# Kernel optimization log

Measured on AMD Instinct MI355X. Metric: run time of the kernel, lower is better.

Reference implementation:

```python
import jax, jax.numpy as jnp
import numpy as np

EPS = 1e-06  # slot-attention renorm epsilon
LN_EPS = 1e-05  # torch LayerNorm default
NUM_ITERS = 3


def layernorm(x, w, b):
    m = jnp.mean(x, axis=-1, keepdims=True)
    v = jnp.mean((x - m) ** 2, axis=-1, keepdims=True)
    return (x - m) * jax.lax.rsqrt(v + LN_EPS) * w + b


def setup_inputs() -> dict:
    key = jax.random.key(0)
    ks = jax.random.split(key, 16)
    B, N, D = 32, 4096, 512
    S, NS, H = 128, 8, 256
    def lin(k, out_f, in_f):
        return jax.random.normal(k, (out_f, in_f), jnp.float32) * (1.0 / np.sqrt(in_f))
    return {
        "inputs": jax.random.normal(ks[0], (B, N, D), jnp.float32),
        "slots_init": jax.random.normal(ks[1], (B, NS, S), jnp.float32),
        "ln_in_w": jnp.ones((D,), jnp.float32), "ln_in_b": jnp.zeros((D,), jnp.float32),
        "ln_slot_w": jnp.ones((S,), jnp.float32), "ln_slot_b": jnp.zeros((S,), jnp.float32),
        "ln_mlp_w": jnp.ones((S,), jnp.float32), "ln_mlp_b": jnp.zeros((S,), jnp.float32),
        "Wq": lin(ks[2], S, S), "Wk": lin(ks[3], S, D), "Wv": lin(ks[4], S, D),
        "gru_Wih": lin(ks[5], 3 * S, S), "gru_Whh": lin(ks[6], 3 * S, S),
        "gru_bih": jnp.zeros((3 * S,), jnp.float32), "gru_bhh": jnp.zeros((3 * S,), jnp.float32),
        "mlp_W1": lin(ks[7], H, S), "mlp_b1": jnp.zeros((H,), jnp.float32),
        "mlp_W2": lin(ks[8], S, H), "mlp_b2": jnp.zeros((S,), jnp.float32),
        "slots_mu": jax.random.normal(ks[9], (1, 1, S), jnp.float32) * 0.1,
        "slots_log_sigma": jax.random.normal(ks[10], (1, 1, S), jnp.float32) * 0.1,
    }


def gru_cell(x, h, Wih, Whh, bih, bhh):
    # PyTorch GRUCell math. x, h: [BS, S]
    S = h.shape[-1]
    gi = x @ Wih.T + bih
    gh = h @ Whh.T + bhh
    i_r, i_z, i_n = gi[:, :S], gi[:, S:2 * S], gi[:, 2 * S:]
    h_r, h_z, h_n = gh[:, :S], gh[:, S:2 * S], gh[:, 2 * S:]
    r = jax.nn.sigmoid(i_r + h_r)
    z = jax.nn.sigmoid(i_z + h_z)
    n = jnp.tanh(i_n + r * h_n)
    return (1.0 - z) * n + z * h


def reference(inputs, slots_init, ln_in_w, ln_in_b, ln_slot_w, ln_slot_b, ln_mlp_w, ln_mlp_b,
              Wq, Wk, Wv, gru_Wih, gru_Whh, gru_bih, gru_bhh,
              mlp_W1, mlp_b1, mlp_W2, mlp_b2, slots_mu, slots_log_sigma):
    B, N, D = inputs.shape
    NS, S = slots_init.shape[1], slots_init.shape[2]
    x = layernorm(inputs, ln_in_w, ln_in_b)
    k = jnp.einsum('bnd,sd->bns', x, Wk)  # [B,N,S]
    v = jnp.einsum('bnd,sd->bns', x, Wv)
    slots = slots_mu + jnp.exp(slots_log_sigma) * slots_init  # [B,NS,S]
    scale = S ** (-0.5)
    for _ in range(NUM_ITERS):
        slots_prev = slots
        q = jnp.einsum('bmd,sd->bms', layernorm(slots, ln_slot_w, ln_slot_b), Wq)  # [B,NS,S]
        attn_logits = scale * jnp.einsum('bns,bms->bnm', k, q)  # [B,N,NS]
        attn = jax.nn.softmax(attn_logits, axis=-1) + EPS
        attn = attn / jnp.sum(attn, axis=1, keepdims=True)  # normalize over inputs
        updates = jnp.einsum('bnm,bns->bms', attn, v)  # [B,NS,S]
        h = gru_cell(updates.reshape(B * NS, S), slots_prev.reshape(B * NS, S),
                     gru_Wih, gru_Whh, gru_bih, gru_bhh).reshape(B, NS, S)
        mlp_out = jnp.maximum(layernorm(h, ln_mlp_w, ln_mlp_b) @ mlp_W1.T + mlp_b1, 0.0) @ mlp_W2.T + mlp_b2
        slots = h + mlp_out
    return slots
```

## Files before the change

kernel.cpp:

```cpp
#include <hip/hip_runtime.h>

typedef __bf16 v8bf __attribute__((ext_vector_type(8)));
typedef __bf16 v4bf __attribute__((ext_vector_type(4)));
typedef float  v4f  __attribute__((ext_vector_type(4)));
typedef unsigned short u16;

#define LN_EPS_F 1e-5f
#define ATTN_EPS 1e-6f

static constexpr int Bsz = 32;
static constexpr int Nn  = 4096;
static constexpr int Dd  = 512;
static constexpr int Ss  = 128;
static constexpr int NSs = 8;
static constexpr int Hh  = 256;
static constexpr int MROWS = Bsz * Nn;

__device__ __forceinline__ void load_lds16(const void* g, void* l) {
    __builtin_amdgcn_global_load_lds(
        (const __attribute__((address_space(1))) void*)g,
        (__attribute__((address_space(3))) void*)l, 16, 0, 0);
}

__global__ __launch_bounds__(256) void k_cast(const float* __restrict__ X,
                                              u16* __restrict__ Xb,
                                              float2* __restrict__ stats) {
    const int wid = threadIdx.x >> 6, lane = threadIdx.x & 63;
    const int row = blockIdx.x * 4 + wid;
    const float4* xp = reinterpret_cast<const float4*>(X + (size_t)row * Dd) + lane * 2;
    float4 a = xp[0];
    float4 b = xp[1];
    float s  = a.x + a.y + a.z + a.w + b.x + b.y + b.z + b.w;
    float s2 = a.x*a.x + a.y*a.y + a.z*a.z + a.w*a.w
             + b.x*b.x + b.y*b.y + b.z*b.z + b.w*b.w;
    v8bf o;
    o[0] = (__bf16)a.x; o[1] = (__bf16)a.y; o[2] = (__bf16)a.z; o[3] = (__bf16)a.w;
    o[4] = (__bf16)b.x; o[5] = (__bf16)b.y; o[6] = (__bf16)b.z; o[7] = (__bf16)b.w;
    *reinterpret_cast<v8bf*>(Xb + (size_t)row * Dd + lane * 8) = o;
#pragma unroll
    for (int off = 32; off > 0; off >>= 1) {
        s  += __shfl_xor(s, off);
        s2 += __shfl_xor(s2, off);
    }
    if (lane == 0) {
        float m = s * (1.0f / Dd);
        float v = s2 * (1.0f / Dd) - m * m;
        stats[row] = make_float2(m, rsqrtf(v + LN_EPS_F));
    }
}

__global__ __launch_bounds__(256) void k_prep(const float* __restrict__ Wk, const float* __restrict__ Wv,
                                              const float* __restrict__ ln_in_w, const float* __restrict__ ln_in_b,
                                              const float* __restrict__ slots_init, const float* __restrict__ mu,
                                              const float* __restrict__ lsig,
                                              u16* __restrict__ Wkvp, float* __restrict__ cb,
                                              float* __restrict__ Scol, float* __restrict__ slots) {
    const int bid = blockIdx.x;
    const int t = threadIdx.x;
    if (bid < 512) {
        int idx = bid * 256 + t;
        int n = idx >> 9, d = idx & 511;
        float w = (n < Ss) ? Wk[n * Dd + d] : Wv[(n - Ss) * Dd + d];
        w *= ln_in_w[d];
        __bf16 bv = (__bf16)w;
        Wkvp[idx] = __builtin_bit_cast(u16, bv);
    } else if (bid < 640) {
        int idx = (bid - 512) * 256 + t;
        int sidx = idx & (Ss - 1);
        slots[idx] = mu[sidx] + expf(lsig[sidx]) * slots_init[idx];
    } else {
        const int wid = t >> 6, lane = t & 63;
        const int rowbase = (bid - 640) * 32 + wid * 8;
        const int d0 = lane * 8;
        float4 lw0 = *reinterpret_cast<const float4*>(ln_in_w + d0);
        float4 lw1 = *reinterpret_cast<const float4*>(ln_in_w + d0 + 4);
        float4 lb0 = *reinterpret_cast<const float4*>(ln_in_b + d0);
        float4 lb1 = *reinterpret_cast<const float4*>(ln_in_b + d0 + 4);
        for (int rr = 0; rr < 8; ++rr) {
            int row = rowbase + rr;
            const float* wrow = (row < Ss) ? (Wk + (size_t)row * Dd)
                                           : (Wv + (size_t)(row - Ss) * Dd);
            float4 w0 = *reinterpret_cast<const float4*>(wrow + d0);
            float4 w1 = *reinterpret_cast<const float4*>(wrow + d0 + 4);
            float accb = lb0.x*w0.x + lb0.y*w0.y + lb0.z*w0.z + lb0.w*w0.w
                       + lb1.x*w1.x + lb1.y*w1.y + lb1.z*w1.z + lb1.w*w1.w;
            float accs = (float)(__bf16)(w0.x*lw0.x) + (float)(__bf16)(w0.y*lw0.y)
                       + (float)(__bf16)(w0.z*lw0.z) + (float)(__bf16)(w0.w*lw0.w)
                       + (float)(__bf16)(w1.x*lw1.x) + (float)(__bf16)(w1.y*lw1.y)
                       + (float)(__bf16)(w1.z*lw1.z) + (float)(__bf16)(w1.w*lw1.w);
#pragma unroll
            for (int off = 32; off > 0; off >>= 1) {
                accb += __shfl_xor(accb, off);
                accs += __shfl_xor(accs, off);
            }
            if (lane == 0) { cb[row] = accb; Scol[row] = accs; }
        }
    }
}

__global__ __launch_bounds__(256, 3) void k_kvgemm(const u16* __restrict__ Xb,
                                                   const float2* __restrict__ stats,
                                                   const u16* __restrict__ Wkvp,
                                                   const float* __restrict__ cb,
                                                   const float* __restrict__ Scol,
                                                   u16* __restrict__ kv) {
    __shared__ __bf16 As[2][128 * 32];
    __shared__ __bf16 Bsh[2][128 * 32];
    __shared__ float2 stats_sh[128];
    const int t    = threadIdx.x;
    const int lane = t & 63;
    const int w    = t >> 6;
    const int wr   = w >> 1;
    const int wc   = w & 1;
    const int lr   = lane & 15;
    const int g    = lane >> 4;
    const size_t m0 = (size_t)blockIdx.x * 128;
    const int n0   = blockIdx.y * 128;

    const int r16  = lane >> 2;
    const int swze = ((lane & 3) ^ ((r16 >> 1) & 3)) * 8;
    const u16* asrc = Xb   + (m0 + w * 32 + r16) * 512 + swze;
    const u16* bsrc = Wkvp + (size_t)(n0 + w * 32 + r16) * 512 + swze;

    if (t < 128) stats_sh[t] = stats[m0 + t];

    const v4f vzero = {0.f, 0.f, 0.f, 0.f};
    v4f acc[4][4];
#pragma unroll
    for (int i = 0; i < 4; ++i)
#pragma unroll
        for (int j = 0; j < 4; ++j) acc[i][j] = vzero;

#define STAGE(buf, kb)                                                          \
    {                                                                           \
        _Pragma("unroll")                                                       \
        for (int i = 0; i < 2; ++i) {                                           \
            load_lds16(asrc + (size_t)i * 16 * 512 + (kb) * 32,                 \
                       &As[buf][(w * 32 + i * 16) * 32]);                       \
            load_lds16(bsrc + (size_t)i * 16 * 512 + (kb) * 32,                 \
                       &Bsh[buf][(w * 32 + i * 16) * 32]);                      \
        }                                                                       \
    }

    STAGE(0, 0);

    const int co = (g ^ ((lr >> 1) & 3)) * 8;
#pragma unroll
    for (int kb = 0; kb < 16; ++kb) {
        const int buf = kb & 1;
        if (kb < 15) STAGE(buf ^ 1, kb + 1);
        if (kb < 15)
            asm volatile("s_waitcnt vmcnt(4)" ::: "memory");
        else
            asm volatile("s_waitcnt vmcnt(0)" ::: "memory");
        __builtin_amdgcn_s_barrier();
        v8bf a[4], b[4];
#pragma unroll
        for (int mi = 0; mi < 4; ++mi)
            a[mi] = *reinterpret_cast<const v8bf*>(
                &As[buf][(wr * 64 + mi * 16 + lr) * 32 + co]);
#pragma unroll
        for (int ni = 0; ni < 4; ++ni)
            b[ni] = *reinterpret_cast<const v8bf*>(
                &Bsh[buf][(wc * 64 + ni * 16 + lr) * 32 + co]);
#pragma unroll
        for (int ni = 0; ni < 4; ++ni)
#pragma unroll
            for (int mi = 0; mi < 4; ++mi)
                acc[mi][ni] = __builtin_amdgcn_mfma_f32_16x16x32_bf16(a[mi], b[ni], acc[mi][ni], 0, 0, 0);
        __builtin_amdgcn_s_barrier();
    }
#undef STAGE
    float Sn[4], cbv[4];
#pragma unroll
    for (int ni = 0; ni < 4; ++ni) {
        int col = n0 + wc * 64 + ni * 16 + lr;
        Sn[ni]  = Scol[col];
        cbv[ni] = cb[col];
    }
#pragma unroll
    for (int mi = 0; mi < 4; ++mi)
#pragma unroll
        for (int j = 0; j < 4; ++j) {
            int rl = wr * 64 + mi * 16 + g * 4 + j;
            float2 st = stats_sh[rl];
            size_t mg = m0 + rl;
#pragma unroll
            for (int ni = 0; ni < 4; ++ni) {
                int col = n0 + wc * 64 + ni * 16 + lr;
                float val = st.y * (acc[mi][ni][j] - st.x * Sn[ni]) + cbv[ni];
                __bf16 bv = (__bf16)val;
                kv[mg * 256 + col] = __builtin_bit_cast(u16, bv);
            }
        }
}

__global__ __launch_bounds__(128) void k_q(const float* __restrict__ slots,
                                           const float* __restrict__ lnw, const float* __restrict__ lnb,
                                           const float* __restrict__ Wq, float* __restrict__ q) {
    __shared__ float xs[128];
    __shared__ float red[4];
    const int t = threadIdx.x;
    const int bm = blockIdx.x;
    float x = slots[bm * 128 + t];
    float s = x, s2 = x * x;
#pragma unroll
    for (int off = 32; off > 0; off >>= 1) { s += __shfl_xor(s, off); s2 += __shfl_xor(s2, off); }
    const int wid = t >> 6, lane = t & 63;
    if (lane == 0) { red[wid * 2] = s; red[wid * 2 + 1] = s2; }
    __syncthreads();
    float S1 = red[0] + red[2], S2 = red[1] + red[3];
    float m = S1 * (1.f / 128.f);
    float rstd = rsqrtf(S2 * (1.f / 128.f) - m * m + LN_EPS_F);
    xs[t] = (x - m) * rstd * lnw[t] + lnb[t];
    __syncthreads();
    const float* wr = Wq + (size_t)t * 128;
    float acc = 0.f;
#pragma unroll 8
    for (int d = 0; d < 128; d += 4) {
        float4 w = *reinterpret_cast<const float4*>(wr + d);
        acc += w.x * xs[d] + w.y * xs[d + 1] + w.z * xs[d + 2] + w.w * xs[d + 3];
    }
    q[bm * 128 + t] = acc * 0.08838834764831845f;
}

__global__ __launch_bounds__(256) void k_attnupd(const u16* __restrict__ kv, const float* __restrict__ q,
                                                 float* __restrict__ upd_part, float* __restrict__ colsum_part) {
    __shared__ float qs[8 * 128];
    __shared__ float at[128][8];
    __shared__ __bf16 vt[128][128];
    __shared__ float colpart[4][8];
    const int b  = blockIdx.y;
    const int ch = blockIdx.x;
    const int t  = threadIdx.x;
    const int lane = t & 63, wv = t >> 6;
    *reinterpret_cast<float4*>(&qs[t * 4]) = *reinterpret_cast<const float4*>(&q[b * 1024 + t * 4]);
    __syncthreads();
    {
        const int rsub = lane >> 4;
        const int csub = (lane & 15) * 8;
#pragma unroll
        for (int p = 0; p < 8; ++p) {
            int row = wv * 32 + p * 4;
            const u16* src = kv + ((size_t)(b * Nn + ch * 128 + row + rsub)) * 256 + 128 + csub;
            load_lds16(src, &vt[row][0]);
        }
    }
    const int nl   = t >> 1;
    const int half = t & 1;
    const u16* krow = kv + ((size_t)(b * Nn + ch * 128 + nl)) * 256 + half * 64;
    float acc[8] = {0.f, 0.f, 0.f, 0.f, 0.f, 0.f, 0.f, 0.f};
#pragma unroll
    for (int c = 0; c < 8; ++c) {
        v8bf kvv = *reinterpret_cast<const v8bf*>(krow + c * 8);
        float kf[8];
#pragma unroll
        for (int j = 0; j < 8; ++j) kf[j] = (float)kvv[j];
#pragma unroll
        for (int m = 0; m < 8; ++m) {
            const float* qrow = &qs[m * 128 + half * 64 + c * 8];
            float aa = 0.f;
#pragma unroll
            for (int j = 0; j < 8; ++j) aa += kf[j] * qrow[j];
            acc[m] += aa;
        }
    }
#pragma unroll
    for (int m = 0; m < 8; ++m) acc[m] += __shfl_xor(acc[m], 1);
    float mx = acc[0];
#pragma unroll
    for (int m = 1; m < 8; ++m) mx = fmaxf(mx, acc[m]);
    float e[8]; float ssum = 0.f;
#pragma unroll
    for (int m = 0; m < 8; ++m) { e[m] = __expf(acc[m] - mx); ssum += e[m]; }
    float inv = 1.0f / ssum;
    float a8[8];
#pragma unroll
    for (int m = 0; m < 8; ++m) a8[m] = e[m] * inv + ATTN_EPS;
    *reinterpret_cast<float4*>(&at[nl][half * 4]) =
        make_float4(a8[half * 4], a8[half * 4 + 1], a8[half * 4 + 2], a8[half * 4 + 3]);
#pragma unroll
    for (int m = 0; m < 8; ++m) {
        float v = a8[m];
#pragma unroll
        for (int off = 32; off > 0; off >>= 1) v += __shfl_xor(v, off);
        if (lane == 0) colpart[wv][m] = v * 0.5f;
    }
    __syncthreads();
    const int m2 = t >> 5;
    const int s0 = (t & 31) * 4;
    float a0 = 0.f, a1 = 0.f, a2 = 0.f, a3 = 0.f;
#pragma unroll 4
    for (int n = 0; n < 128; ++n) {
        float a = at[n][m2];
        v4bf vvv = *reinterpret_cast<const v4bf*>(&vt[n][s0]);
        a0 += a * (float)vvv[0];
        a1 += a * (float)vvv[1];
        a2 += a * (float)vvv[2];
        a3 += a * (float)vvv[3];
    }
    *reinterpret_cast<float4*>(upd_part + ((size_t)(b * 32 + ch) * 8 + m2) * 128 + s0) =
        make_float4(a0, a1, a2, a3);
    if (t < 8)
        colsum_part[(b * 32 + ch) * 8 + t] =
            colpart[0][t] + colpart[1][t] + colpart[2][t] + colpart[3][t];
}

__global__ __launch_bounds__(256) void k_finishq(const float* __restrict__ upd_part,
                                                 const float* __restrict__ colsum_part,
                                                 const float* __restrict__ slots_in,
                                                 const float* __restrict__ Wih, const float* __restrict__ Whh,
                                                 const float* __restrict__ bih, const float* __restrict__ bhh,
                                                 const float* __restrict__ lnw, const float* __restrict__ lnb,
                                                 const float* __restrict__ W1, const float* __restrict__ b1,
                                                 const float* __restrict__ W2, const float* __restrict__ b2,
                                                 const float* __restrict__ lnsw, const float* __restrict__ lnsb,
                                                 const float* __restrict__ Wq,
                                                 float* __restrict__ slots_out, float* __restrict__ qout) {
    __shared__ float us[128], sp[128], hnorm[128], qsrc[128], act[256];
    __shared__ float upart[2][128];
    __shared__ float gpart[2][6][128];
    __shared__ float p2[2][128];
    __shared__ float qpart[2][128];
    __shared__ float red[4];
    __shared__ float csum_sh;
    const int t   = threadIdx.x;
    const int tid = t & 127, half = t >> 7;
    const int bm  = blockIdx.x;
    const int b = bm >> 3, m = bm & 7;
    if (t < 64) {
        float v = (t < 32) ? colsum_part[(b * 32 + t) * 8 + m] : 0.f;
#pragma unroll
        for (int off = 32; off > 0; off >>= 1) v += __shfl_xor(v, off);
        if (t == 0) csum_sh = v;
    }
    float u = 0.f;
#pragma unroll 4
    for (int chk = half * 16; chk < half * 16 + 16; ++chk)
        u += upd_part[((size_t)(b * 32 + chk) * 8 + m) * 128 + tid];
    upart[half][tid] = u;
    if (half == 0) sp[tid] = slots_in[bm * 128 + tid];
    __syncthreads();
    if (half == 0) us[tid] = (upart[0][tid] + upart[1][tid]) * (1.f / csum_sh);
    __syncthreads();
    {
        const int d0g = half * 64;
        float a_r = 0.f, a_z = 0.f, a_n = 0.f, b_r = 0.f, b_z = 0.f, b_n = 0.f;
        const float* Wr = Wih + (size_t)tid * 128 + d0g;
        const float* Wz = Wih + (size_t)(128 + tid) * 128 + d0g;
        const float* Wn = Wih + (size_t)(256 + tid) * 128 + d0g;
        const float* Vr = Whh + (size_t)tid * 128 + d0g;
        const float* Vz = Whh + (size_t)(128 + tid) * 128 + d0g;
        const float* Vn = Whh + (size_t)(256 + tid) * 128 + d0g;
#pragma unroll 4
        for (int d = 0; d < 64; d += 4) {
            float u0 = us[d0g + d], u1 = us[d0g + d + 1], u2 = us[d0g + d + 2], u3 = us[d0g + d + 3];
            float p0 = sp[d0g + d], p1 = sp[d0g + d + 1], p2_ = sp[d0g + d + 2], p3 = sp[d0g + d + 3];
            float4 w;
            w = *reinterpret_cast<const float4*>(Wr + d); a_r += w.x*u0 + w.y*u1 + w.z*u2 + w.w*u3;
            w = *reinterpret_cast<const float4*>(Wz + d); a_z += w.x*u0 + w.y*u1 + w.z*u2 + w.w*u3;
            w = *reinterpret_cast<const float4*>(Wn + d); a_n += w.x*u0 + w.y*u1 + w.z*u2 + w.w*u3;
            w = *reinterpret_cast<const float4*>(Vr + d); b_r += w.x*p0 + w.y*p1 + w.z*p2_ + w.w*p3;
            w = *reinterpret_cast<const float4*>(Vz + d); b_z += w.x*p0 + w.y*p1 + w.z*p2_ + w.w*p3;
            w = *reinterpret_cast<const float4*>(Vn + d); b_n += w.x*p0 + w.y*p1 + w.z*p2_ + w.w*p3;
        }
        gpart[half][0][tid] = a_r; gpart[half][1][tid] = a_z; gpart[half][2][tid] = a_n;
        gpart[half][3][tid] = b_r; gpart[half][4][tid] = b_z; gpart[half][5][tid] = b_n;
    }
    __syncthreads();
    float gir = bih[tid]       + gpart[0][0][tid] + gpart[1][0][tid];
    float giz = bih[128 + tid] + gpart[0][1][tid] + gpart[1][1][tid];
    float gin = bih[256 + tid] + gpart[0][2][tid] + gpart[1][2][tid];
    float ghr = bhh[tid]       + gpart[0][3][tid] + gpart[1][3][tid];
    float ghz = bhh[128 + tid] + gpart[0][4][tid] + gpart[1][4][tid];
    float ghn = bhh[256 + tid] + gpart[0][5][tid] + gpart[1][5][tid];
    float h0 = sp[tid];
    float r  = 1.f / (1.f + __expf(-(gir + ghr)));
    float z  = 1.f / (1.f + __expf(-(giz + ghz)));
    float nn = tanhf(gin + r * ghn);
    float h  = (1.f - z) * nn + z * h0;
    if (half == 0) {
        float s = h, s2 = h * h;
#pragma unroll
        for (int off = 32; off > 0; off >>= 1) { s += __shfl_xor(s, off); s2 += __shfl_xor(s2, off); }
        if ((t & 63) == 0) { red[(tid >> 6) * 2] = s; red[(tid >> 6) * 2 + 1] = s2; }
    }
    __syncthreads();
    {
        float S1 = red[0] + red[2], S2 = red[1] + red[3];
        float mean = S1 * (1.f / Ss);
        float rstd = rsqrtf(S2 * (1.f / Ss) - mean * mean + LN_EPS_F);
        if (half == 0) hnorm[tid] = (h - mean) * rstd * lnw[tid] + lnb[tid];
    }
    __syncthreads();
    {
        float a = b1[t];
        const float* w1r = W1 + (size_t)t * 128;
#pragma unroll 4
        for (int d = 0; d < 128; d += 4) {
            float4 w = *reinterpret_cast<const float4*>(w1r + d);
            a += w.x * hnorm[d] + w.y * hnorm[d + 1] + w.z * hnorm[d + 2] + w.w * hnorm[d + 3];
        }
        act[t] = fmaxf(a, 0.f);
    }
    __syncthreads();
    {
        float o = 0.f;
        const int j0 = half * 128;
        const float* w2r = W2 + (size_t)tid * 256 + j0;
#pragma unroll 4
        for (int j = 0; j < 128; j += 4) {
            float4 w = *reinterpret_cast<const float4*>(w2r + j);
            o += w.x * act[j0 + j] + w.y * act[j0 + j + 1] + w.z * act[j0 + j + 2] + w.w * act[j0 + j + 3];
        }
        p2[half][tid] = o;
    }
    __syncthreads();
    float snew = h + b2[tid] + p2[0][tid] + p2[1][tid];
    if (half == 0) slots_out[bm * 128 + tid] = snew;
    if (half == 0) {
        float s = snew, s2 = snew * snew;
#pragma unroll
        for (int off = 32; off > 0; off >>= 1) { s += __shfl_xor(s, off); s2 += __shfl_xor(s2, off); }
        if ((t & 63) == 0) { red[(tid >> 6) * 2] = s; red[(tid >> 6) * 2 + 1] = s2; }
    }
    __syncthreads();
    {
        float T1 = red[0] + red[2], T2 = red[1] + red[3];
        float m2 = T1 * (1.f / Ss);
        float rstd2 = rsqrtf(T2 * (1.f / Ss) - m2 * m2 + LN_EPS_F);
        if (half == 0) qsrc[tid] = (snew - m2) * rstd2 * lnsw[tid] + lnsb[tid];
    }
    __syncthreads();
    {
        float qa = 0.f;
        const int d0g = half * 64;
        const float* wr = Wq + (size_t)tid * 128 + d0g;
#pragma unroll 4
        for (int d = 0; d < 64; d += 4) {
            float4 w = *reinterpret_cast<const float4*>(wr + d);
            qa += w.x * qsrc[d0g + d] + w.y * qsrc[d0g + d + 1] + w.z * qsrc[d0g + d + 2] + w.w * qsrc[d0g + d + 3];
        }
        qpart[half][tid] = qa;
    }
    __syncthreads();
    if (half == 0)
        qout[bm * 128 + tid] = (qpart[0][tid] + qpart[1][tid]) * 0.08838834764831845f;
}

extern "C" void kernel_launch(void* const* d_in, const int* in_sizes, int n_in,
                              void* d_out, int out_size, void* d_ws, size_t ws_size,
                              hipStream_t stream) {
    const float* X          = (const float*)d_in[0];
    const float* slots_init = (const float*)d_in[1];
    const float* ln_in_w    = (const float*)d_in[2];
    const float* ln_in_b    = (const float*)d_in[3];
    const float* ln_slot_w  = (const float*)d_in[4];
    const float* ln_slot_b  = (const float*)d_in[5];
    const float* ln_mlp_w   = (const float*)d_in[6];
    const float* ln_mlp_b   = (const float*)d_in[7];
    const float* Wq         = (const float*)d_in[8];
    const float* Wk         = (const float*)d_in[9];
    const float* Wv         = (const float*)d_in[10];
    const float* gWih       = (const float*)d_in[11];
    const float* gWhh       = (const float*)d_in[12];
    const float* gbih       = (const float*)d_in[13];
    const float* gbhh       = (const float*)d_in[14];
    const float* W1         = (const float*)d_in[15];
    const float* b1         = (const float*)d_in[16];
    const float* W2         = (const float*)d_in[17];
    const float* b2         = (const float*)d_in[18];
    const float* mu         = (const float*)d_in[19];
    const float* lsig       = (const float*)d_in[20];

    char* p = (char*)d_ws;
    u16*    Wkvp        = (u16*)p;    p += (size_t)256 * 512 * sizeof(u16);
    float*  cb          = (float*)p;  p += 256 * sizeof(float);
    float*  Scol        = (float*)p;  p += 256 * sizeof(float);
    float*  slots       = (float*)p;  p += 32 * 8 * 128 * sizeof(float);
    float*  qbuf        = (float*)p;  p += 32 * 8 * 128 * sizeof(float);
    float*  colsum_part = (float*)p;  p += 32 * 32 * 8 * sizeof(float);
    float*  upd_part    = (float*)p;  p += (size_t)32 * 32 * 8 * 128 * sizeof(float);
    u16*    kv          = (u16*)p;    p += (size_t)MROWS * 256 * sizeof(u16);
    u16*    Xb          = (u16*)p;    p += (size_t)MROWS * Dd * sizeof(u16);
    float2* stats       = (float2*)p; p += (size_t)MROWS * sizeof(float2);

    k_cast<<<MROWS / 4, 256, 0, stream>>>(X, Xb, stats);
    k_prep<<<648, 256, 0, stream>>>(Wk, Wv, ln_in_w, ln_in_b, slots_init, mu, lsig,
                                    Wkvp, cb, Scol, slots);
    k_kvgemm<<<dim3(MROWS / 128, 2), 256, 0, stream>>>(Xb, stats, Wkvp, cb, Scol, kv);
    k_q<<<256, 128, 0, stream>>>(slots, ln_slot_w, ln_slot_b, Wq, qbuf);

    for (int it = 0; it < 3; ++it) {
        k_attnupd<<<dim3(32, 32), 256, 0, stream>>>(kv, qbuf, upd_part, colsum_part);
        k_finishq<<<256, 256, 0, stream>>>(upd_part, colsum_part, slots,
                                           gWih, gWhh, gbih, gbhh,
                                           ln_mlp_w, ln_mlp_b, W1, b1, W2, b2,
                                           ln_slot_w, ln_slot_b, Wq,
                                           (it == 2) ? (float*)d_out : slots, qbuf);
    }
}
```

Baseline: 322.1 us.

## Fuse input fp32-to-bf16 cast and LayerNorm stats into KV GEMM

Removes the separate cast kernel and the bf16 copy of the input. The KV GEMM now stages fp32 input tiles straight into LDS, accumulates row sum and sum-of-squares while building bf16 MFMA operands, and derives the LayerNorm stats in its epilogue. The grid is transposed so the two N-tiles sharing an M-tile run adjacently and can reuse the fp32 rows in L2. The cost is double the LDS for the A tile, which may limit occupancy, plus per-iteration conversion ALU work, and each fp32 row may be read twice from global memory.

```diff
diff --git a/kernel.cpp b/kernel.cpp
--- a/kernel.cpp
+++ b/kernel.cpp
@@ -20,33 +20,6 @@
     __builtin_amdgcn_global_load_lds(
         (const __attribute__((address_space(1))) void*)g,
         (__attribute__((address_space(3))) void*)l, 16, 0, 0);
-}
-
-__global__ __launch_bounds__(256) void k_cast(const float* __restrict__ X,
-                                              u16* __restrict__ Xb,
-                                              float2* __restrict__ stats) {
-    const int wid = threadIdx.x >> 6, lane = threadIdx.x & 63;
-    const int row = blockIdx.x * 4 + wid;
-    const float4* xp = reinterpret_cast<const float4*>(X + (size_t)row * Dd) + lane * 2;
-    float4 a = xp[0];
-    float4 b = xp[1];
-    float s  = a.x + a.y + a.z + a.w + b.x + b.y + b.z + b.w;
-    float s2 = a.x*a.x + a.y*a.y + a.z*a.z + a.w*a.w
-             + b.x*b.x + b.y*b.y + b.z*b.z + b.w*b.w;
-    v8bf o;
-    o[0] = (__bf16)a.x; o[1] = (__bf16)a.y; o[2] = (__bf16)a.z; o[3] = (__bf16)a.w;
-    o[4] = (__bf16)b.x; o[5] = (__bf16)b.y; o[6] = (__bf16)b.z; o[7] = (__bf16)b.w;
-    *reinterpret_cast<v8bf*>(Xb + (size_t)row * Dd + lane * 8) = o;
-#pragma unroll
-    for (int off = 32; off > 0; off >>= 1) {
-        s  += __shfl_xor(s, off);
-        s2 += __shfl_xor(s2, off);
-    }
-    if (lane == 0) {
-        float m = s * (1.0f / Dd);
-        float v = s2 * (1.0f / Dd) - m * m;
-        stats[row] = make_float2(m, rsqrtf(v + LN_EPS_F));
-    }
 }
 
 __global__ __launch_bounds__(256) void k_prep(const float* __restrict__ Wk, const float* __restrict__ Wv,
@@ -98,13 +71,12 @@
     }
 }
 
-__global__ __launch_bounds__(256, 3) void k_kvgemm(const u16* __restrict__ Xb,
-                                                   const float2* __restrict__ stats,
+__global__ __launch_bounds__(256, 3) void k_kvgemm(const float* __restrict__ X,
                                                    const u16* __restrict__ Wkvp,
                                                    const float* __restrict__ cb,
                                                    const float* __restrict__ Scol,
                                                    u16* __restrict__ kv) {
-    __shared__ __bf16 As[2][128 * 32];
+    __shared__ float  As[2][128 * 32];
     __shared__ __bf16 Bsh[2][128 * 32];
     __shared__ float2 stats_sh[128];
     const int t    = threadIdx.x;
@@ -114,15 +86,13 @@
     const int wc   = w & 1;
     const int lr   = lane & 15;
     const int g    = lane >> 4;
-    const size_t m0 = (size_t)blockIdx.x * 128;
-    const int n0   = blockIdx.y * 128;
-
-    const int r16  = lane >> 2;
-    const int swze = ((lane & 3) ^ ((r16 >> 1) & 3)) * 8;
-    const u16* asrc = Xb   + (m0 + w * 32 + r16) * 512 + swze;
-    const u16* bsrc = Wkvp + (size_t)(n0 + w * 32 + r16) * 512 + swze;
-
-    if (t < 128) stats_sh[t] = stats[m0 + t];
+    const int n0   = blockIdx.x * 128;
+    const size_t m0 = (size_t)blockIdx.y * 128;
+
+    const float* asrc = X + (m0 + w * 32 + (lane >> 3)) * 512
+                          + (size_t)(((lane & 7) ^ (lane >> 3)) * 4);
+    const u16* bsrc = Wkvp + (size_t)(n0 + w * 32 + (lane >> 2)) * 512
+                           + (size_t)((((lane & 3) ^ ((lane >> 3) & 3))) * 8);
 
     const v4f vzero = {0.f, 0.f, 0.f, 0.f};
     v4f acc[4][4];
@@ -130,39 +100,56 @@
     for (int i = 0; i < 4; ++i)
 #pragma unroll
         for (int j = 0; j < 4; ++j) acc[i][j] = vzero;
+    float s1[4] = {0.f, 0.f, 0.f, 0.f};
+    float s2[4] = {0.f, 0.f, 0.f, 0.f};
 
 #define STAGE(buf, kb)                                                          \
     {                                                                           \
         _Pragma("unroll")                                                       \
-        for (int i = 0; i < 2; ++i) {                                           \
-            load_lds16(asrc + (size_t)i * 16 * 512 + (kb) * 32,                 \
-                       &As[buf][(w * 32 + i * 16) * 32]);                       \
+        for (int i = 0; i < 4; ++i)                                             \
+            load_lds16(asrc + (size_t)i * 8 * 512 + (kb) * 32,                  \
+                       &As[buf][(w * 32 + i * 8) * 32]);                        \
+        _Pragma("unroll")                                                       \
+        for (int i = 0; i < 2; ++i)                                             \
             load_lds16(bsrc + (size_t)i * 16 * 512 + (kb) * 32,                 \
                        &Bsh[buf][(w * 32 + i * 16) * 32]);                      \
-        }                                                                       \
     }
 
     STAGE(0, 0);
 
-    const int co = (g ^ ((lr >> 1) & 3)) * 8;
+    const int pa_lo = ((2 * g)     ^ (lr & 7)) * 4;
+    const int pa_hi = ((2 * g + 1) ^ (lr & 7)) * 4;
+    const int cob   = (g ^ ((lr >> 1) & 3)) * 8;
+
 #pragma unroll
     for (int kb = 0; kb < 16; ++kb) {
         const int buf = kb & 1;
         if (kb < 15) STAGE(buf ^ 1, kb + 1);
         if (kb < 15)
-            asm volatile("s_waitcnt vmcnt(4)" ::: "memory");
+            asm volatile("s_waitcnt vmcnt(6)" ::: "memory");
         else
             asm volatile("s_waitcnt vmcnt(0)" ::: "memory");
         __builtin_amdgcn_s_barrier();
+        const float*  ab = &As[buf][0];
+        const __bf16* bb = &Bsh[buf][0];
         v8bf a[4], b[4];
 #pragma unroll
-        for (int mi = 0; mi < 4; ++mi)
-            a[mi] = *reinterpret_cast<const v8bf*>(
-                &As[buf][(wr * 64 + mi * 16 + lr) * 32 + co]);
+        for (int mi = 0; mi < 4; ++mi) {
+            const float* arow = ab + (wr * 64 + mi * 16 + lr) * 32;
+            float4 lo = *reinterpret_cast<const float4*>(arow + pa_lo);
+            float4 hi = *reinterpret_cast<const float4*>(arow + pa_hi);
+            s1[mi] += lo.x + lo.y + lo.z + lo.w + hi.x + hi.y + hi.z + hi.w;
+            s2[mi] += lo.x*lo.x + lo.y*lo.y + lo.z*lo.z + lo.w*lo.w
+                    + hi.x*hi.x + hi.y*hi.y + hi.z*hi.z + hi.w*hi.w;
+            v8bf av;
+            av[0] = (__bf16)lo.x; av[1] = (__bf16)lo.y; av[2] = (__bf16)lo.z; av[3] = (__bf16)lo.w;
+            av[4] = (__bf16)hi.x; av[5] = (__bf16)hi.y; av[6] = (__bf16)hi.z; av[7] = (__bf16)hi.w;
+            a[mi] = av;
+        }
 #pragma unroll
         for (int ni = 0; ni < 4; ++ni)
             b[ni] = *reinterpret_cast<const v8bf*>(
-                &Bsh[buf][(wc * 64 + ni * 16 + lr) * 32 + co]);
+                bb + (wc * 64 + ni * 16 + lr) * 32 + cob);
 #pragma unroll
         for (int ni = 0; ni < 4; ++ni)
 #pragma unroll
@@ -171,6 +158,20 @@
         __builtin_amdgcn_s_barrier();
     }
 #undef STAGE
+#pragma unroll
+    for (int mi = 0; mi < 4; ++mi) {
+        s1[mi] += __shfl_xor(s1[mi], 16); s1[mi] += __shfl_xor(s1[mi], 32);
+        s2[mi] += __shfl_xor(s2[mi], 16); s2[mi] += __shfl_xor(s2[mi], 32);
+    }
+    if (g == 0 && (w & 1) == 0) {
+#pragma unroll
+        for (int mi = 0; mi < 4; ++mi) {
+            float mn = s1[mi] * (1.f / Dd);
+            float vv = s2[mi] * (1.f / Dd) - mn * mn;
+            stats_sh[wr * 64 + mi * 16 + lr] = make_float2(mn, rsqrtf(vv + LN_EPS_F));
+        }
+    }
+    __syncthreads();
     float Sn[4], cbv[4];
 #pragma unroll
     for (int ni = 0; ni < 4; ++ni) {
@@ -482,13 +483,10 @@
     float*  colsum_part = (float*)p;  p += 32 * 32 * 8 * sizeof(float);
     float*  upd_part    = (float*)p;  p += (size_t)32 * 32 * 8 * 128 * sizeof(float);
     u16*    kv          = (u16*)p;    p += (size_t)MROWS * 256 * sizeof(u16);
-    u16*    Xb          = (u16*)p;    p += (size_t)MROWS * Dd * sizeof(u16);
-    float2* stats       = (float2*)p; p += (size_t)MROWS * sizeof(float2);
-
-    k_cast<<<MROWS / 4, 256, 0, stream>>>(X, Xb, stats);
+
     k_prep<<<648, 256, 0, stream>>>(Wk, Wv, ln_in_w, ln_in_b, slots_init, mu, lsig,
                                     Wkvp, cb, Scol, slots);
-    k_kvgemm<<<dim3(MROWS / 128, 2), 256, 0, stream>>>(Xb, stats, Wkvp, cb, Scol, kv);
+    k_kvgemm<<<dim3(2, MROWS / 128), 256, 0, stream>>>(X, Wkvp, cb, Scol, kv);
     k_q<<<256, 128, 0, stream>>>(slots, ln_slot_w, ln_slot_b, Wq, qbuf);
 
     for (int it = 0; it < 3; ++it) {
```

New measurement: 944.8 us. 2.93x slower.
